# Kernel tuning notes

Hardware: AMD Instinct MI355X
Metric: run time of the kernel (lower is better)

Reference implementation:

```python
import jax, jax.numpy as jnp
import numpy as np

EPS = 1e-5

def conv2d(x, w, b, stride, pad):
    out = jax.lax.conv_general_dilated(x, w, (stride, stride), [(pad, pad), (pad, pad)],
                                       dimension_numbers=('NCHW', 'OIHW', 'NCHW'))
    return out + b[None, :, None, None]

def instance_norm(x):
    # nn.InstanceNorm2d default: affine=False, eps=1e-5, per (N,C) over (H,W)
    m = jnp.mean(x, axis=(2, 3), keepdims=True)
    v = jnp.var(x, axis=(2, 3), keepdims=True)
    return (x - m) * jax.lax.rsqrt(v + EPS)

def deform_conv2d(x, offset, mask, w, b, stride, pad):
    # x: [N,Cin,H,W]; offset: [N,2K,Ho,Wo] as [dy(K);dx(K)]; mask: [N,K,Ho,Wo]
    N, Cin, H, W = x.shape
    Cout, _, kh, kw = w.shape
    K = kh * kw
    Ho, Wo = mask.shape[2], mask.shape[3]
    oy, ox = offset[:, :K], offset[:, K:]
    ky, kx = jnp.meshgrid(jnp.arange(kh), jnp.arange(kw), indexing='ij')
    ky = ky.reshape(K).astype(x.dtype)
    kx = kx.reshape(K).astype(x.dtype)
    base_y = (jnp.arange(Ho) * stride - pad).astype(x.dtype)
    base_x = (jnp.arange(Wo) * stride - pad).astype(x.dtype)
    # sampling coords [N,K,Ho,Wo]
    py = base_y[None, None, :, None] + ky[None, :, None, None] + oy
    px = base_x[None, None, None, :] + kx[None, :, None, None] + ox
    y0 = jnp.floor(py)
    x0 = jnp.floor(px)
    wy = (py - y0)[:, None]  # [N,1,K,Ho,Wo]
    wx = (px - x0)[:, None]
    flat = x.reshape(N, Cin, H * W)

    def sample(yi, xi):
        valid = ((yi >= 0) & (yi <= H - 1) & (xi >= 0) & (xi <= W - 1)).astype(x.dtype)
        yc = jnp.clip(yi, 0, H - 1).astype(jnp.int32)
        xc = jnp.clip(xi, 0, W - 1).astype(jnp.int32)
        idx = yc * W + xc  # [N,K,Ho,Wo]
        vals = jax.vmap(lambda f, i: f[:, i])(flat, idx)  # [N,Cin,K,Ho,Wo]
        return vals * valid[:, None]

    v00 = sample(y0, x0)
    v01 = sample(y0, x0 + 1)
    v10 = sample(y0 + 1, x0)
    v11 = sample(y0 + 1, x0 + 1)
    samp = (v00 * (1 - wy) * (1 - wx) + v01 * (1 - wy) * wx
            + v10 * wy * (1 - wx) + v11 * wy * wx)
    samp = samp * mask[:, None]  # modulated (DCNv2)
    out = jnp.einsum('nckhw,ock->nohw', samp, w.reshape(Cout, Cin, K))
    return out + b[None, :, None, None]

def mdcp(x, off_w, off_b, dcn_w, dcn_b, stride, pad):
    # ModulatedDeformConvPack.forward with input_offset == input_real == x
    o = conv2d(x, off_w, off_b, stride, pad)
    K = o.shape[1] // 3
    o1, o2, m = o[:, :K], o[:, K:2 * K], o[:, 2 * K:]
    offset = jnp.concatenate([o1, o2], axis=1)
    mask = jax.nn.sigmoid(m)
    return deform_conv2d(x, offset, mask, dcn_w, dcn_b, stride, pad)

def res_block(x, w1, b1, w2, b2):
    # MUNIT-style ResBlock: [reflect-pad conv3x3, IN, ReLU] -> [reflect-pad conv3x3, IN] + skip
    h = jnp.pad(x, ((0, 0), (0, 0), (1, 1), (1, 1)), mode='reflect')
    h = jax.nn.relu(instance_norm(conv2d(h, w1, b1, 1, 0)))
    h = jnp.pad(h, ((0, 0), (0, 0), (1, 1), (1, 1)), mode='reflect')
    h = instance_norm(conv2d(h, w2, b2, 1, 0))
    return x + h

def setup_inputs() -> dict:
    key = jax.random.key(0)
    ks = jax.random.split(key, 32)
    N, H, W = 2, 256, 256

    def wconv(k, shape, scale=None):
        if scale is None:
            scale = 1.0 / np.sqrt(shape[1] * shape[2] * shape[3])
        return jax.random.normal(k, shape, jnp.float32) * scale

    def bias(k, n, scale=0.01):
        return jax.random.normal(k, (n,), jnp.float32) * scale

    inp = {}
    inp['x'] = jax.random.normal(ks[0], (N, 3, H, W), jnp.float32)
    # offset/mask convs: small weights (sub-pixel offsets; trained-from-zero in original)
    inp['off1_w'] = wconv(ks[1], (147, 3, 7, 7), 0.01)
    inp['off1_b'] = bias(ks[2], 147)
    inp['dcn1_w'] = wconv(ks[3], (64, 3, 7, 7))
    inp['dcn1_b'] = bias(ks[4], 64)
    inp['off2_w'] = wconv(ks[5], (48, 64, 4, 4), 0.01)
    inp['off2_b'] = bias(ks[6], 48)
    inp['dcn2_w'] = wconv(ks[7], (128, 64, 4, 4))
    inp['dcn2_b'] = bias(ks[8], 128)
    inp['off3_w'] = wconv(ks[9], (48, 128, 4, 4), 0.01)
    inp['off3_b'] = bias(ks[10], 48)
    inp['dcn3_w'] = wconv(ks[11], (256, 128, 4, 4))
    inp['dcn3_b'] = bias(ks[12], 256)
    for i, base in ((1, 13), (2, 17)):
        inp[f'rb{i}_w1'] = wconv(ks[base], (256, 256, 3, 3))
        inp[f'rb{i}_b1'] = bias(ks[base + 1], 256)
        inp[f'rb{i}_w2'] = wconv(ks[base + 2], (256, 256, 3, 3))
        inp[f'rb{i}_b2'] = bias(ks[base + 3], 256)
    return inp

def reference(x, off1_w, off1_b, dcn1_w, dcn1_b, off2_w, off2_b, dcn2_w, dcn2_b,
              off3_w, off3_b, dcn3_w, dcn3_b,
              rb1_w1, rb1_b1, rb1_w2, rb1_b2, rb2_w1, rb2_b1, rb2_w2, rb2_b2):
    h = jax.nn.relu(instance_norm(mdcp(x, off1_w, off1_b, dcn1_w, dcn1_b, 1, 3)))
    skip1 = h
    h = jax.nn.relu(instance_norm(mdcp(h, off2_w, off2_b, dcn2_w, dcn2_b, 2, 1)))
    skip2 = h
    h = jax.nn.relu(instance_norm(mdcp(h, off3_w, off3_b, dcn3_w, dcn3_b, 2, 1)))
    h = res_block(h, rb1_w1, rb1_b1, rb1_w2, rb1_b2)
    h = res_block(h, rb2_w1, rb2_b1, rb2_w2, rb2_b2)
    return (h, skip1, skip2)
```

## Files before the change

kernel.cpp:

```cpp
#include <hip/hip_runtime.h>
#include <hip/hip_bf16.h>
#include <math.h>

#define TPB 256
typedef __hip_bfloat16 bf16;
typedef short bf16x8 __attribute__((ext_vector_type(8)));
typedef float f32x4 __attribute__((ext_vector_type(4)));

constexpr long BIASF  = 0;
constexpr long RB1W1T = 2048;
constexpr long RB1W2T = 591872;
constexpr long RB2W1T = 1181696;
constexpr long RB2W2T = 1771520;
constexpr long FB     = 2361344;
constexpr long WB1OT  = 2361344;
constexpr long WB1DT  = 2382956;
constexpr long WO2T   = 2392364;
constexpr long WB2T   = 2441516;
constexpr long WO3T   = 2572588;
constexpr long WB3T   = 2670892;
constexpr long OFFB   = 3221504;
constexpr long H3F    = 4458496;
constexpr long CLBUF  = 5523456;
constexpr long PST1   = 7620608;
constexpr long PST2   = 7653376;
constexpr long OFF1B = 0,   DCN1B = 147;
constexpr long OFF2B = 211, DCN2B = 259;
constexpr long OFF3B = 387, DCN3B = 435;
constexpr long RB1B1 = 691, RB1B2 = 947;
constexpr long RB2B1 = 1203, RB2B2 = 1459;

template<int BF>
__device__ __forceinline__ float ldT(const void* p, long i) {
    if (BF) {
        unsigned short h = ((const unsigned short*)p)[i];
        return __uint_as_float(((unsigned int)h) << 16);
    }
    return ((const float*)p)[i];
}
template<int BF>
__device__ __forceinline__ void stT(void* p, long i, float v) {
    if (BF) ((bf16*)p)[i] = __float2bfloat16(v);
    else    ((float*)p)[i] = v;
}
__device__ __forceinline__ float bitsToF(unsigned short h) {
    return __uint_as_float(((unsigned int)h) << 16);
}
__device__ __forceinline__ unsigned short fToBits(float v) {
    bf16 h = __float2bfloat16(v);
    return *(unsigned short*)&h;
}

__global__ void detect_kernel(const void* __restrict__ x, int* __restrict__ flag) {
    if (threadIdx.x == 0 && blockIdx.x == 0) {
        const unsigned short* u = (const unsigned short*)x;
        int sane = 0;
        for (int i = 0; i < 256; ++i) {
            float v = bitsToF(u[i]);
            float a = fabsf(v);
            if (a > 0.0009f && a < 1100.f) ++sane;
        }
        *flag = (sane >= 224) ? 1 : 0;
    }
}

struct PtrPack { const void* p[20]; };

template<int BF>
__device__ void repack_all_body(PtrPack pp, float* __restrict__ fw)
{
    constexpr int  bcum  [11] = {0,147,211,259,387,435,691,947,1203,1459,1715};
    int j0 = blockIdx.x * 1024 + threadIdx.x * 4;
    #pragma unroll
    for (int q = 0; q < 4; ++q) {
        int j = j0 + q;
        if (j < 1715) {
            int v = 0;
            #pragma unroll
            for (int s = 1; s < 10; ++s) if (j >= bcum[s]) v = s;
            fw[BIASF + j] = ldT<BF>(pp.p[10 + v], j - bcum[v]);
        }
    }
}
__global__ __launch_bounds__(TPB) void repack_all_kernel(
    PtrPack pp, float* fw, const int* dflag) {
    if (*dflag) repack_all_body<1>(pp, fw);
    else        repack_all_body<0>(pp, fw);
}

__global__ __launch_bounds__(TPB) void repack_dcn_kernel(
    const void* __restrict__ w2, const void* __restrict__ w3,
    const void* __restrict__ w1o, const void* __restrict__ w1d,
    const void* __restrict__ w2o, const void* __restrict__ w3o,
    float* __restrict__ fw, const int* __restrict__ dflag)
{
    int bf = *dflag;
    unsigned short* wb2 = (unsigned short*)(fw + WB2T);
    unsigned short* wb3 = (unsigned short*)(fw + WB3T);
    unsigned short* wb1o = (unsigned short*)(fw + WB1OT);
    unsigned short* wb1d = (unsigned short*)(fw + WB1DT);
    unsigned short* wb2o = (unsigned short*)(fw + WO2T);
    unsigned short* wb3o = (unsigned short*)(fw + WO3T);
    int b = blockIdx.x;
    if (b < 128) {
        int e0 = b * 1024 + threadIdx.x * 4;
        #pragma unroll
        for (int j = 0; j < 4; ++j) {
            int e = e0 + j;
            int co = e >> 10, rem = e & 1023, k = rem >> 6, ci = rem & 63;
            long si = ((long)(co * 64 + ci)) * 16 + k;
            float v = bf ? ldT<1>(w2, si) : ldT<0>(w2, si);
            wb2[e] = fToBits(v);
        }
    } else if (b < 640) {
        int e0 = (b - 128) * 1024 + threadIdx.x * 4;
        #pragma unroll
        for (int j = 0; j < 4; ++j) {
            int e = e0 + j;
            int co = e >> 11, rem = e & 2047, k = rem >> 7, ci = rem & 127;
            long si = ((long)(co * 128 + ci)) * 16 + k;
            float v = bf ? ldT<1>(w3, si) : ldT<0>(w3, si);
            wb3[e] = fToBits(v);
        }
    } else if (b < 665) {
        int e0 = (b - 640) * 1024 + threadIdx.x * 4;
        #pragma unroll
        for (int j = 0; j < 4; ++j) {
            int e = e0 + j;
            int co = e / 160, k = e - co * 160;
            float v = 0.f;
            if (co < 147 && k < 147) {
                long si = (long)co * 147 + k;
                v = bf ? ldT<1>(w1o, si) : ldT<0>(w1o, si);
            }
            wb1o[e] = fToBits(v);
        }
    } else if (b < 675) {
        int e0 = (b - 665) * 1024 + threadIdx.x * 4;
        #pragma unroll
        for (int j = 0; j < 4; ++j) {
            int e = e0 + j;
            int co = e / 160, k = e - co * 160;
            float v = 0.f;
            if (k < 147) {
                long si = (long)co * 147 + k;
                v = bf ? ldT<1>(w1d, si) : ldT<0>(w1d, si);
            }
            wb1d[e] = fToBits(v);
        }
    } else if (b < 739) {
        int e0 = (b - 675) * 1024 + threadIdx.x * 4;
        #pragma unroll
        for (int j = 0; j < 4; ++j) {
            int e = e0 + j;
            int co = e >> 10, rem = e & 1023, k = rem >> 6, ci = rem & 63;
            float v = 0.f;
            if (co < 48) {
                long si = ((long)(co * 64 + ci)) * 16 + k;
                v = bf ? ldT<1>(w2o, si) : ldT<0>(w2o, si);
            }
            wb2o[e] = fToBits(v);
        }
    } else {
        int e0 = (b - 739) * 1024 + threadIdx.x * 4;
        #pragma unroll
        for (int j = 0; j < 4; ++j) {
            int e = e0 + j;
            int co = e >> 11, rem = e & 2047, k = rem >> 7, ci = rem & 127;
            float v = 0.f;
            if (co < 48) {
                long si = ((long)(co * 128 + ci)) * 16 + k;
                v = bf ? ldT<1>(w3o, si) : ldT<0>(w3o, si);
            }
            wb3o[e] = fToBits(v);
        }
    }
}

struct RbPack { const void* src[4]; };
__global__ __launch_bounds__(TPB) void repack_rb_kernel(
    RbPack rp, float* fw, const int* dflag)
{
    __shared__ unsigned short lw[4 * 2304];
    int b = blockIdx.x;
    int ten = b >> 6;
    int co0 = (b & 63) * 4;
    const void* src = rp.src[ten];
    const long dstOff[4] = {RB1W1T, RB1W2T, RB2W1T, RB2W2T};
    unsigned short* dst = (unsigned short*)(fw + dstOff[ten]);
    int bf = *dflag;
    int t = threadIdx.x;
    for (int e = t; e < 4 * 2304; e += TPB) {
        int coL = e / 2304, i = e - coL * 2304;
        long si = (long)(co0 + coL) * 2304 + i;
        float v = bf ? ldT<1>(src, si) : ldT<0>(src, si);
        lw[e] = fToBits(v);
    }
    __syncthreads();
    for (int e = t; e < 9216; e += TPB) {
        int ci = e & 255, coL = (e >> 8) & 3, q = e >> 10;
        dst[((long)q * 256 + co0 + coL) * 256 + ci] = lw[coL * 2304 + ci * 9 + q];
    }
}

template<int BF>
__device__ void x_to_cl4_body(const void* __restrict__ x, unsigned short* __restrict__ x4)
{
    long gid = (long)blockIdx.x * TPB + threadIdx.x;
    int n = (int)(gid >> 16); int p = (int)(gid & 65535);
    long xb = (long)n * 3 * 65536 + p;
    unsigned c0 = fToBits(ldT<BF>(x, xb));
    unsigned c1 = fToBits(ldT<BF>(x, xb + 65536));
    unsigned c2 = fToBits(ldT<BF>(x, xb + 131072));
    uint2 v; v.x = c0 | (c1 << 16); v.y = c2;
    *(uint2*)&x4[gid * 4] = v;
}
__global__ __launch_bounds__(TPB) void x_to_cl4_kernel(
    const void* x, unsigned short* x4, const int* dflag)
{
    if (*dflag) x_to_cl4_body<1>(x, x4);
    else        x_to_cl4_body<0>(x, x4);
}

template<int BF>
__device__ void layer1_mfma_body(
    const unsigned short* __restrict__ x4all, const unsigned short* __restrict__ wo,
    const unsigned short* __restrict__ wd, const float* __restrict__ bias1,
    const float* __restrict__ bias2, void* __restrict__ out, long obase,
    float* xs, unsigned short* A, float* offs)
{
    int b = blockIdx.x;
    int n = b >> 11;
    int ho = (b >> 3) & 255;
    int wo0 = (b & 7) << 5;
    const unsigned short* x4 = x4all + ((long)n << 16) * 4;
    int t = threadIdx.x;

    for (int e = t; e < 7 * 40; e += TPB) {
        int cc = e % 40, rr = e / 40;
        int yy = ho - 3 + rr; int xx = wo0 - 3 + cc;
        float c0 = 0.f, c1 = 0.f, c2 = 0.f;
        if (cc < 38 && yy >= 0 && yy < 256 && xx >= 0 && xx < 256) {
            uint2 v = *(const uint2*)&x4[((long)yy * 256 + xx) * 4];
            c0 = bitsToF((unsigned short)(v.x & 0xffff));
            c1 = bitsToF((unsigned short)(v.x >> 16));
            c2 = bitsToF((unsigned short)(v.y & 0xffff));
        }
        xs[(0 * 7 + rr) * 40 + cc] = c0;
        xs[(1 * 7 + rr) * 40 + cc] = c1;
        xs[(2 * 7 + rr) * 40 + cc] = c2;
    }
    __syncthreads();

    for (int e = t; e < 5120; e += TPB) {
        int kin = e & 31, m = (e >> 5) & 31, kc = e >> 10;
        int k = kc * 32 + kin;
        float v = 0.f;
        if (k < 147) {
            int ci = k / 49, q = k - ci * 49;
            int ky = q / 7, kx = q - ky * 7;
            v = xs[(ci * 7 + ky) * 40 + m + kx];
        }
        A[kc * 1024 + m * 32 + kin] = fToBits(v);
    }
    __syncthreads();

    int wv = t >> 6, lane = t & 63;
    int quad = lane >> 4, l16 = lane & 15;
    int mt = wv & 1, ntb = wv >> 1;

    {
        f32x4 acc[5];
        #pragma unroll
        for (int j = 0; j < 5; ++j) acc[j] = (f32x4){0.f, 0.f, 0.f, 0.f};
        #pragma unroll
        for (int kc = 0; kc < 5; ++kc) {
            bf16x8 a = *(const bf16x8*)&A[(kc * 32 + mt * 16 + l16) * 32 + quad * 8];
            #pragma unroll
            for (int j = 0; j < 5; ++j) {
                int ch = (ntb + 2 * j) * 16 + l16;
                bf16x8 bw = *(const bf16x8*)&wo[ch * 160 + kc * 32 + quad * 8];
                acc[j] = __builtin_amdgcn_mfma_f32_16x16x32_bf16(a, bw, acc[j], 0, 0, 0);
            }
        }
        #pragma unroll
        for (int j = 0; j < 5; ++j) {
            int ch = (ntb + 2 * j) * 16 + l16;
            if (ch < 147) {
                float bv = bias1[ch];
                #pragma unroll
                for (int reg = 0; reg < 4; ++reg) {
                    int m = mt * 16 + quad * 4 + reg;
                    offs[ch * 33 + m] = acc[j][reg] + bv;
                }
            }
        }
    }
    __syncthreads();

    for (int e = t; e < 49 * 32; e += TPB) {
        int p = e & 31; int k = e >> 5;
        float oy = offs[k * 33 + p];
        float ox = offs[(49 + k) * 33 + p];
        float mr = offs[(98 + k) * 33 + p];
        float m = 1.f / (1.f + expf(-mr));
        float py = (float)(ho - 3 + k / 7) + oy;
        float px = (float)(wo0 + p - 3 + k % 7) + ox;
        float y0f = floorf(py), x0f = floorf(px);
        float wy = py - y0f, wx = px - x0f;
        int y0 = (int)y0f, x0 = (int)x0f;
        bool yv0 = (y0 >= 0) && (y0 < 256);
        bool yv1 = (y0 + 1 >= 0) && (y0 + 1 < 256);
        bool xv0 = (x0 >= 0) && (x0 < 256);
        bool xv1 = (x0 + 1 >= 0) && (x0 + 1 < 256);
        int y0c = min(max(y0, 0), 255), y1c = min(max(y0 + 1, 0), 255);
        int x0c = min(max(x0, 0), 255), x1c = min(max(x0 + 1, 0), 255);
        float w00 = (yv0 && xv0) ? (1.f - wy) * (1.f - wx) * m : 0.f;
        float w01 = (yv0 && xv1) ? (1.f - wy) * wx * m : 0.f;
        float w10 = (yv1 && xv0) ? wy * (1.f - wx) * m : 0.f;
        float w11 = (yv1 && xv1) ? wy * wx * m : 0.f;
        uint2 a00 = *(const uint2*)&x4[((long)y0c * 256 + x0c) * 4];
        uint2 a01 = *(const uint2*)&x4[((long)y0c * 256 + x1c) * 4];
        uint2 a10 = *(const uint2*)&x4[((long)y1c * 256 + x0c) * 4];
        uint2 a11 = *(const uint2*)&x4[((long)y1c * 256 + x1c) * 4];
        float s0 = w00 * bitsToF((unsigned short)(a00.x & 0xffff))
                 + w01 * bitsToF((unsigned short)(a01.x & 0xffff))
                 + w10 * bitsToF((unsigned short)(a10.x & 0xffff))
                 + w11 * bitsToF((unsigned short)(a11.x & 0xffff));
        float s1 = w00 * bitsToF((unsigned short)(a00.x >> 16))
                 + w01 * bitsToF((unsigned short)(a01.x >> 16))
                 + w10 * bitsToF((unsigned short)(a10.x >> 16))
                 + w11 * bitsToF((unsigned short)(a11.x >> 16));
        float s2 = w00 * bitsToF((unsigned short)(a00.y & 0xffff))
                 + w01 * bitsToF((unsigned short)(a01.y & 0xffff))
                 + w10 * bitsToF((unsigned short)(a10.y & 0xffff))
                 + w11 * bitsToF((unsigned short)(a11.y & 0xffff));
        offs[k * 33 + p] = s0;
        offs[(49 + k) * 33 + p] = s1;
        offs[(98 + k) * 33 + p] = s2;
    }
    __syncthreads();

    for (int e = t; e < 5120; e += TPB) {
        int kin = e & 31, m = (e >> 5) & 31, kc = e >> 10;
        int k = kc * 32 + kin;
        float v = 0.f;
        if (k < 147) v = offs[k * 33 + m];
        A[kc * 1024 + m * 32 + kin] = fToBits(v);
    }
    __syncthreads();

    f32x4 acc2[2];
    acc2[0] = (f32x4){0.f, 0.f, 0.f, 0.f};
    acc2[1] = (f32x4){0.f, 0.f, 0.f, 0.f};
    #pragma unroll
    for (int kc = 0; kc < 5; ++kc) {
        bf16x8 a = *(const bf16x8*)&A[(kc * 32 + mt * 16 + l16) * 32 + quad * 8];
        #pragma unroll
        for (int j = 0; j < 2; ++j) {
            int co = (ntb + 2 * j) * 16 + l16;
            bf16x8 bw = *(const bf16x8*)&wd[co * 160 + kc * 32 + quad * 8];
            acc2[j] = __builtin_amdgcn_mfma_f32_16x16x32_bf16(a, bw, acc2[j], 0, 0, 0);
        }
    }
    #pragma unroll
    for (int j = 0; j < 2; ++j) {
        int co = (ntb + 2 * j) * 16 + l16;
        float bv = bias2[co];
        #pragma unroll
        for (int reg = 0; reg < 4; ++reg) {
            int wox = wo0 + mt * 16 + quad * 4 + reg;
            long oi = obase + ((long)(n * 64 + co) * 256 + ho) * 256 + wox;
            stT<BF>(out, oi, acc2[j][reg] + bv);
        }
    }
}

__global__ __launch_bounds__(TPB) void layer1_mfma_kernel(
    const unsigned short* x4, const unsigned short* wo, const unsigned short* wd,
    const float* bias1, const float* bias2, void* out, long obase, const int* dflag)
{
    __shared__ __align__(16) float xs[3 * 7 * 40];
    __shared__ __align__(16) unsigned short A[5120];
    __shared__ __align__(16) float offs[147 * 33];
    if (*dflag) layer1_mfma_body<1>(x4, wo, wd, bias1, bias2, out, obase, xs, A, offs);
    else        layer1_mfma_body<0>(x4, wo, wd, bias1, bias2, out, obase, xs, A, offs);
}

template<int CIN, int HH, int WW, int HO, int WO>
__global__ __launch_bounds__(TPB) void offconv_mfma_kernel(
    const unsigned short* __restrict__ xcl, const unsigned short* __restrict__ wb,
    const float* __restrict__ bias_f, float* __restrict__ out)
{
    constexpr int S   = 16 * CIN;
    constexpr int KL  = 512 / CIN;
    constexpr int NCH = 16 / KL;
    constexpr int CH8 = CIN / 8;
    constexpr int UN  = (KL * 16 * CH8) / TPB;
    constexpr int TILES = (HO * WO) / 16;

    __shared__ int tp[256];
    __shared__ __align__(16) unsigned short smp[16 * 512];

    int tile = blockIdx.x % TILES;
    int n    = blockIdx.x / TILES;
    int lp0  = tile * 16;

    {
        int pr = threadIdx.x;
        int k = pr >> 4, p = pr & 15;
        int lp = lp0 + p;
        int ho = lp / WO, wo = lp - ho * WO;
        int yy = ho * 2 - 1 + (k >> 2);
        int xx = wo * 2 - 1 + (k & 3);
        bool valid = (yy >= 0) && (yy < HH) && (xx >= 0) && (xx < WW);
        tp[pr] = valid ? (yy * WW + xx) * CIN : -1;
    }

    int wv = threadIdx.x >> 6, lane = threadIdx.x & 63;
    int quad = lane >> 4, l16 = lane & 15;
    const unsigned short* xn = xcl + (long)n * HH * WW * CIN;

    f32x4 acc = (f32x4){0.f, 0.f, 0.f, 0.f};

    for (int ch = 0; ch < NCH; ++ch) {
        __syncthreads();
        #pragma unroll
        for (int u = 0; u < UN; ++u) {
            int e   = u * TPB + threadIdx.x;
            int prl = e / CH8;
            int ci  = (e - prl * CH8) * 8;
            int pi  = ch * (KL * 16) + prl;
            int kl = prl >> 4, p = prl & 15;
            int t0 = tp[pi];
            uint4 v = {0u, 0u, 0u, 0u};
            if (t0 >= 0) v = *(const uint4*)(xn + t0 + ci);
            int il = kl * CIN + ci;
            *(uint4*)&smp[((il >> 5) * 16 + p) * 32 + (il & 31)] = v;
        }
        __syncthreads();
        #pragma unroll 4
        for (int kk = 0; kk < 16; ++kk) {
            bf16x8 a = *(const bf16x8*)&smp[(kk * 16 + l16) * 32 + quad * 8];
            int co = wv * 16 + l16;
            bf16x8 b = *(const bf16x8*)&wb[(long)co * S + ch * 512 + kk * 32 + quad * 8];
            acc = __builtin_amdgcn_mfma_f32_16x16x32_bf16(a, b, acc, 0, 0, 0);
        }
    }

    int co = wv * 16 + l16;
    if (co < 48) {
        float bv = bias_f[co];
        #pragma unroll
        for (int reg = 0; reg < 4; ++reg) {
            int lp = lp0 + quad * 4 + reg;
            int ho = lp / WO, wo = lp - ho * WO;
            out[((long)(n * 48 + co) * HO + ho) * WO + wo] = acc[reg] + bv;
        }
    }
}

template<int C>
__global__ __launch_bounds__(TPB) void nchw_to_cl_kernel(
    const void* __restrict__ in, long ibase, unsigned short* __restrict__ out,
    int HW, const int* __restrict__ dflag)
{
    __shared__ unsigned short tile[C * 65];
    int bf = *dflag;
    int n   = (blockIdx.x * 64) / HW;
    int px0 = (blockIdx.x * 64) % HW;
    for (int e = threadIdx.x; e < C * 64; e += TPB) {
        int c = e >> 6, p = e & 63;
        long si = ibase + (long)(n * C + c) * HW + px0 + p;
        float v = bf ? ldT<1>(in, si) : ldT<0>(in, si);
        tile[c * 65 + p] = fToBits(v);
    }
    __syncthreads();
    for (int e = threadIdx.x; e < C * 64; e += TPB) {
        int p = e / C, c = e - p * C;
        out[((long)n * HW + px0 + p) * C + c] = tile[c * 65 + p];
    }
}

template<int MODE, int CIN, int COUT, int NWAVES, int HH, int WW, int HO, int WO>
__global__ __launch_bounds__(NWAVES * 64) void deform_mfma_kernel(
    const unsigned short* __restrict__ xcl, const float* __restrict__ off,
    const unsigned short* __restrict__ wb, const float* __restrict__ bias_f,
    void* __restrict__ outp, long obase, const int* __restrict__ dflag)
{
    constexpr int TPBk = NWAVES * 64;
    constexpr int S    = 16 * CIN;
    constexpr int KL   = 512 / CIN;
    constexpr int NCH  = 16 / KL;
    constexpr int CH8  = CIN / 8;
    constexpr int ITER = (KL * 16 * CH8) / TPBk;
    constexpr int TILES = (HO * WO) / 16;

    __shared__ __align__(16) int tpw[256][8];
    __shared__ __align__(16) unsigned short smp[16 * 512];

    int tile = blockIdx.x % TILES;
    int n    = blockIdx.x / TILES;
    int lp0  = tile * 16;
    int tid  = threadIdx.x;

    if (tid < 256) {
        int pr = tid;
        int k = pr >> 4, p = pr & 15;
        int lp = lp0 + p;
        int ho = lp / WO, wo = lp - ho * WO;
        long plane = (long)HO * WO;
        const float* offn = off + (long)n * 48 * plane;
        float oy = offn[(long)k * plane + lp];
        float ox = offn[(long)(16 + k) * plane + lp];
        float mr = offn[(long)(32 + k) * plane + lp];
        float m = 1.f / (1.f + expf(-mr));
        float py = (float)(ho * 2 - 1 + (k >> 2)) + oy;
        float px = (float)(wo * 2 - 1 + (k & 3)) + ox;
        float y0f = floorf(py), x0f = floorf(px);
        float wy = py - y0f, wx = px - x0f;
        int y0 = (int)y0f, x0 = (int)x0f;
        bool yv0 = (y0 >= 0) && (y0 < HH);
        bool yv1 = (y0 + 1 >= 0) && (y0 + 1 < HH);
        bool xv0 = (x0 >= 0) && (x0 < WW);
        bool xv1 = (x0 + 1 >= 0) && (x0 + 1 < WW);
        int y0c = min(max(y0, 0), HH - 1), y1c = min(max(y0 + 1, 0), HH - 1);
        int x0c = min(max(x0, 0), WW - 1), x1c = min(max(x0 + 1, 0), WW - 1);
        tpw[pr][0] = (y0c * WW + x0c) * CIN;
        tpw[pr][1] = (y0c * WW + x1c) * CIN;
        tpw[pr][2] = (y1c * WW + x0c) * CIN;
        tpw[pr][3] = (y1c * WW + x1c) * CIN;
        tpw[pr][4] = __float_as_int((yv0 && xv0) ? (1.f - wy) * (1.f - wx) * m : 0.f);
        tpw[pr][5] = __float_as_int((yv0 && xv1) ? (1.f - wy) * wx * m : 0.f);
        tpw[pr][6] = __float_as_int((yv1 && xv0) ? wy * (1.f - wx) * m : 0.f);
        tpw[pr][7] = __float_as_int((yv1 && xv1) ? wy * wx * m : 0.f);
    }

    int wv = tid >> 6, lane = tid & 63;
    int quad = lane >> 4, l16 = lane & 15;
    int cb = (wv & 3) * 32 + (wv >> 2) * (COUT / 2);
    const unsigned short* xn = xcl + (long)n * HH * WW * CIN;

    f32x4 acc[2];
    acc[0] = (f32x4){0.f, 0.f, 0.f, 0.f};
    acc[1] = (f32x4){0.f, 0.f, 0.f, 0.f};

    for (int ch = 0; ch < NCH; ++ch) {
        __syncthreads();
        #pragma unroll
        for (int it = 0; it < ITER; ++it) {
            int e   = it * TPBk + tid;
            int prl = e / CH8;
            int ci  = (e - prl * CH8) * 8;
            int pi  = ch * (KL * 16) + prl;
            const int4   tp4 = *(const int4*)&tpw[pi][0];
            const float4 tw4 = *(const float4*)&tpw[pi][4];
            uint4 u0 = *(const uint4*)(xn + tp4.x + ci);
            uint4 u1 = *(const uint4*)(xn + tp4.y + ci);
            uint4 u2 = *(const uint4*)(xn + tp4.z + ci);
            uint4 u3 = *(const uint4*)(xn + tp4.w + ci);
            float r[8];
            #pragma unroll
            for (int jj = 0; jj < 8; ++jj) {
                unsigned w0 = ((const unsigned*)&u0)[jj >> 1];
                unsigned w1 = ((const unsigned*)&u1)[jj >> 1];
                unsigned w2 = ((const unsigned*)&u2)[jj >> 1];
                unsigned w3 = ((const unsigned*)&u3)[jj >> 1];
                int sh = (jj & 1) << 4;
                r[jj] = tw4.x * bitsToF((unsigned short)(w0 >> sh))
                      + tw4.y * bitsToF((unsigned short)(w1 >> sh))
                      + tw4.z * bitsToF((unsigned short)(w2 >> sh))
                      + tw4.w * bitsToF((unsigned short)(w3 >> sh));
            }
            uint4 ov;
            ((unsigned*)&ov)[0] = (unsigned)fToBits(r[0]) | ((unsigned)fToBits(r[1]) << 16);
            ((unsigned*)&ov)[1] = (unsigned)fToBits(r[2]) | ((unsigned)fToBits(r[3]) << 16);
            ((unsigned*)&ov)[2] = (unsigned)fToBits(r[4]) | ((unsigned)fToBits(r[5]) << 16);
            ((unsigned*)&ov)[3] = (unsigned)fToBits(r[6]) | ((unsigned)fToBits(r[7]) << 16);
            int il = (prl >> 4) * CIN + ci;
            int p  = prl & 15;
            *(uint4*)&smp[((il >> 5) * 16 + p) * 32 + (il & 31)] = ov;
        }
        __syncthreads();
        #pragma unroll 4
        for (int kk = 0; kk < 16; ++kk) {
            bf16x8 a = *(const bf16x8*)&smp[(kk * 16 + l16) * 32 + quad * 8];
            #pragma unroll
            for (int f = 0; f < 2; ++f) {
                int co = cb + f * 16 + l16;
                bf16x8 b = *(const bf16x8*)&wb[(long)co * S + ch * 512 + kk * 32 + quad * 8];
                acc[f] = __builtin_amdgcn_mfma_f32_16x16x32_bf16(a, b, acc[f], 0, 0, 0);
            }
        }
    }

    if (MODE == 1) {
        unsigned short* oCL = (unsigned short*)outp;
        #pragma unroll
        for (int f = 0; f < 2; ++f) {
            int co = cb + f * 16 + l16;
            float bv = bias_f[co];
            #pragma unroll
            for (int reg = 0; reg < 4; ++reg) {
                int lp = lp0 + quad * 4 + reg;
                oCL[((long)n * HO * WO + lp) * COUT + co] = fToBits(acc[f][reg] + bv);
            }
        }
    } else {
        int bf = *dflag;
        #pragma unroll
        for (int f = 0; f < 2; ++f) {
            int co = cb + f * 16 + l16;
            float bv = bias_f[co];
            #pragma unroll
            for (int reg = 0; reg < 4; ++reg) {
                int lp = lp0 + quad * 4 + reg;
                int ho = lp / WO, wo = lp - ho * WO;
                long oi = obase + ((long)(n * COUT + co) * HO + ho) * WO + wo;
                if (bf) stT<1>(outp, oi, acc[f][reg] + bv);
                else    stT<0>(outp, oi, acc[f][reg] + bv);
            }
        }
    }
}

__global__ __launch_bounds__(TPB) void resconv_mfma_kernel(
    const unsigned short* __restrict__ X, const unsigned short* __restrict__ W,
    const float* __restrict__ bias_f, bf16* __restrict__ Y)
{
    __shared__ __align__(16) unsigned short xs[3 * 66 * 64];
    int b = blockIdx.x;
    int coO = b & 7, r = (b >> 3) & 63, n = b >> 9;
    int t = threadIdx.x;
    int wv = t >> 6;
    int lane = t & 63;
    int quad = lane >> 4, l16 = lane & 15;
    int rows[3];
    rows[0] = (r == 0) ? 1 : r - 1;
    rows[1] = r;
    rows[2] = (r == 63) ? 62 : r + 1;

    f32x4 acc[2];
    acc[0] = (f32x4){0.f, 0.f, 0.f, 0.f};
    acc[1] = (f32x4){0.f, 0.f, 0.f, 0.f};

    long xbase = (long)n * 4096 * 256;

    for (int ci0 = 0; ci0 < 256; ci0 += 64) {
        __syncthreads();
        for (int e = t; e < 3 * 66 * 8; e += TPB) {
            int oct = e & 7;
            int col = (e >> 3) % 66;
            int ky  = e / (66 * 8);
            int gx = col - 1;
            gx = (gx < 0) ? 1 : ((gx > 63) ? 62 : gx);
            bf16x8 v = *(const bf16x8*)&X[xbase + ((long)rows[ky] * 64 + gx) * 256 + ci0 + oct * 8];
            int slot = oct ^ (col & 7);
            *(bf16x8*)&xs[((ky * 66 + col) << 6) + slot * 8] = v;
        }
        __syncthreads();
        #pragma unroll
        for (int q = 0; q < 9; ++q) {
            int ky = q / 3, kx = q % 3;
            int col = wv * 16 + l16 + kx;
            int base = (ky * 66 + col) << 6;
            #pragma unroll
            for (int kh = 0; kh < 2; ++kh) {
                int slot = (kh * 4 + quad) ^ (col & 7);
                bf16x8 a = *(const bf16x8*)&xs[base + slot * 8];
                #pragma unroll
                for (int ct = 0; ct < 2; ++ct) {
                    int co = coO * 32 + ct * 16 + l16;
                    bf16x8 bw = *(const bf16x8*)&W[((long)q * 256 + co) * 256 + ci0 + kh * 32 + quad * 8];
                    acc[ct] = __builtin_amdgcn_mfma_f32_16x16x32_bf16(a, bw, acc[ct], 0, 0, 0);
                }
            }
        }
    }

    long ybase = ((long)n * 4096 + (long)r * 64) * 256;
    #pragma unroll
    for (int ct = 0; ct < 2; ++ct) {
        int co = coO * 32 + ct * 16 + l16;
        float bv = bias_f[co];
        #pragma unroll
        for (int reg = 0; reg < 4; ++reg) {
            int px = wv * 16 + quad * 4 + reg;
            Y[ybase + (long)px * 256 + co] = __float2bfloat16(acc[ct][reg] + bv);
        }
    }
}

__global__ __launch_bounds__(TPB) void cl_stats_kernel(
    const unsigned short* __restrict__ X, float* __restrict__ psum, float* __restrict__ psq)
{
    int blk = blockIdx.x;
    int chunk = blk & 63, n = blk >> 6;
    int co = threadIdx.x;
    float s = 0.f, sq = 0.f;
    const unsigned short* p = X + ((long)n * 4096 + chunk * 64) * 256 + co;
    #pragma unroll 8
    for (int i = 0; i < 64; ++i) {
        float v = bitsToF(p[(long)i * 256]);
        s += v; sq += v * v;
    }
    psum[(n * 64 + chunk) * 256 + co] = s;
    psq [(n * 64 + chunk) * 256 + co] = sq;
}

__device__ __forceinline__ void cl_load_stats(
    const float* psum, const float* psq, int n, float* mv, float* iv)
{
    int t = threadIdx.x;
    float s = 0.f, sq = 0.f;
    #pragma unroll 8
    for (int c = 0; c < 64; ++c) {
        s  += psum[(n * 64 + c) * 256 + t];
        sq += psq [(n * 64 + c) * 256 + t];
    }
    float mean = s / 4096.f;
    mv[t] = mean;
    iv[t] = rsqrtf(sq / 4096.f - mean * mean + 1e-5f);
    __syncthreads();
}

__global__ __launch_bounds__(TPB) void cl_apply_kernel(
    unsigned short* __restrict__ X, const float* __restrict__ psum,
    const float* __restrict__ psq, int relu)
{
    __shared__ float mv[256], iv[256];
    int y = blockIdx.x & 63, n = blockIdx.x >> 6;
    cl_load_stats(psum, psq, n, mv, iv);
    unsigned* row = (unsigned*)(X + ((long)n * 4096 + y * 64) * 256);
    for (int e = threadIdx.x; e < 8192; e += TPB) {
        int co = (e * 2) & 255;
        unsigned u = row[e];
        float v0 = (bitsToF((unsigned short)(u & 0xffff)) - mv[co]) * iv[co];
        float v1 = (bitsToF((unsigned short)(u >> 16)) - mv[co + 1]) * iv[co + 1];
        if (relu) { v0 = fmaxf(v0, 0.f); v1 = fmaxf(v1, 0.f); }
        row[e] = (unsigned)fToBits(v0) | ((unsigned)fToBits(v1) << 16);
    }
}

__global__ __launch_bounds__(TPB) void cl_apply_add_kernel(
    const unsigned short* __restrict__ T, unsigned short* __restrict__ H,
    const float* __restrict__ psum, const float* __restrict__ psq)
{
    __shared__ float mv[256], iv[256];
    int y = blockIdx.x & 63, n = blockIdx.x >> 6;
    cl_load_stats(psum, psq, n, mv, iv);
    long base = ((long)n * 4096 + y * 64) * 256;
    const unsigned* tr = (const unsigned*)(T + base);
    unsigned* hr = (unsigned*)(H + base);
    for (int e = threadIdx.x; e < 8192; e += TPB) {
        int co = (e * 2) & 255;
        unsigned ut = tr[e], uh = hr[e];
        float v0 = bitsToF((unsigned short)(uh & 0xffff))
                 + (bitsToF((unsigned short)(ut & 0xffff)) - mv[co]) * iv[co];
        float v1 = bitsToF((unsigned short)(uh >> 16))
                 + (bitsToF((unsigned short)(ut >> 16)) - mv[co + 1]) * iv[co + 1];
        hr[e] = (unsigned)fToBits(v0) | ((unsigned)fToBits(v1) << 16);
    }
}

__global__ __launch_bounds__(TPB) void cl_apply_final_kernel(
    const unsigned short* __restrict__ T, const unsigned short* __restrict__ H,
    void* __restrict__ outp, const float* __restrict__ psum,
    const float* __restrict__ psq, const int* __restrict__ dflag)
{
    __shared__ float mv[256], iv[256];
    int y = blockIdx.x & 63, n = blockIdx.x >> 6;
    cl_load_stats(psum, psq, n, mv, iv);
    int bf = *dflag;
    int x = threadIdx.x & 63, cg = threadIdx.x >> 6;
    for (int co = cg; co < 256; co += 4) {
        long cli = ((long)(n * 64 + y) * 64 + x) * 256 + co;
        float v = bitsToF(H[cli]) + (bitsToF(T[cli]) - mv[co]) * iv[co];
        long oi = (((long)(n * 256 + co)) * 64 + y) * 64 + x;
        if (bf) ((bf16*)outp)[oi] = __float2bfloat16(v);
        else    ((float*)outp)[oi] = v;
    }
}

__device__ __forceinline__ void reduce2(float& sum, float& sq, float* s1, float* s2)
{
    for (int off = 32; off; off >>= 1) {
        sum += __shfl_down(sum, off, 64);
        sq  += __shfl_down(sq,  off, 64);
    }
    int nw = blockDim.x >> 6;
    int wid = threadIdx.x >> 6;
    if ((threadIdx.x & 63) == 0) { s1[wid] = sum; s2[wid] = sq; }
    __syncthreads();
    sum = 0.f; sq = 0.f;
    for (int w = 0; w < nw; ++w) { sum += s1[w]; sq += s2[w]; }
}

__global__ void instnorm_kernel(
    void* __restrict__ buf, long base0, const int* __restrict__ dflag,
    int HW, int relu)
{
    __shared__ float s1[16], s2[16];
    int bf = *dflag;
    long base = base0 + (long)blockIdx.x * HW;
    float sum = 0.f, sq = 0.f;
    for (int i = threadIdx.x; i < HW; i += blockDim.x) {
        float v = bf ? bitsToF(((const unsigned short*)buf)[base + i])
                     : ((const float*)buf)[base + i];
        sum += v; sq += v * v;
    }
    reduce2(sum, sq, s1, s2);
    float mean = sum / HW;
    float inv = rsqrtf(sq / HW - mean * mean + 1e-5f);
    for (int i = threadIdx.x; i < HW; i += blockDim.x) {
        float v = bf ? bitsToF(((const unsigned short*)buf)[base + i])
                     : ((const float*)buf)[base + i];
        v = (v - mean) * inv;
        if (relu) v = fmaxf(v, 0.f);
        if (bf) ((bf16*)buf)[base + i] = __float2bfloat16(v);
        else    ((float*)buf)[base + i] = v;
    }
}

extern "C" void kernel_launch(void* const* d_in, const int* in_sizes, int n_in,
                              void* d_out, int out_size, void* d_ws, size_t ws_size,
                              hipStream_t stream) {
    const void* x = d_in[0];

    const long SKIP1 = 2097152;
    const long SKIP2 = 10485760;

    int* dflag = (int*)d_ws;
    float* fw = (float*)((char*)d_ws + 64);

    unsigned short* t1 = (unsigned short*)(fw + FB);
    unsigned short* t2 = (unsigned short*)(fw + FB + 1048576);
    unsigned short* h3 = (unsigned short*)(fw + H3F);
    float* offb = fw + OFFB;
    unsigned short* x4 = (unsigned short*)(fw + OFFB);
    float* psum = fw + PST1;
    float* psq  = fw + PST2;
    unsigned short* clbuf = (unsigned short*)(fw + CLBUF);
    const unsigned short* wb1o = (const unsigned short*)(fw + WB1OT);
    const unsigned short* wb1d = (const unsigned short*)(fw + WB1DT);
    const unsigned short* wb2o = (const unsigned short*)(fw + WO2T);
    const unsigned short* wb3o = (const unsigned short*)(fw + WO3T);
    const unsigned short* wb2 = (const unsigned short*)(fw + WB2T);
    const unsigned short* wb3 = (const unsigned short*)(fw + WB3T);
    const unsigned short* rbw1 = (const unsigned short*)(fw + RB1W1T);
    const unsigned short* rbw2 = (const unsigned short*)(fw + RB1W2T);
    const unsigned short* rbw3 = (const unsigned short*)(fw + RB2W1T);
    const unsigned short* rbw4 = (const unsigned short*)(fw + RB2W2T);

    detect_kernel<<<1, 64, 0, stream>>>(x, dflag);

    PtrPack pp;
    for (int i = 0; i < 10; ++i) pp.p[i] = nullptr;
    pp.p[10] = d_in[2];  pp.p[11] = d_in[4];  pp.p[12] = d_in[6];  pp.p[13] = d_in[8];
    pp.p[14] = d_in[10]; pp.p[15] = d_in[12]; pp.p[16] = d_in[14]; pp.p[17] = d_in[16];
    pp.p[18] = d_in[18]; pp.p[19] = d_in[20];
    repack_all_kernel<<<2, TPB, 0, stream>>>(pp, fw, dflag);
    repack_dcn_kernel<<<867, TPB, 0, stream>>>(
        d_in[7], d_in[11], d_in[1], d_in[3], d_in[5], d_in[9], fw, dflag);
    RbPack rp;
    rp.src[0] = d_in[13]; rp.src[1] = d_in[15]; rp.src[2] = d_in[17]; rp.src[3] = d_in[19];
    repack_rb_kernel<<<256, TPB, 0, stream>>>(rp, fw, dflag);

    x_to_cl4_kernel<<<512, TPB, 0, stream>>>(x, x4, dflag);
    layer1_mfma_kernel<<<4096, TPB, 0, stream>>>(
        x4, wb1o, wb1d, fw + OFF1B, fw + DCN1B, d_out, SKIP1, dflag);
    instnorm_kernel<<<128, 1024, 0, stream>>>(d_out, SKIP1, dflag, 65536, 1);
    nchw_to_cl_kernel<64><<<2048, TPB, 0, stream>>>(d_out, SKIP1, clbuf, 65536, dflag);

    offconv_mfma_kernel<64, 256, 256, 128, 128><<<2048, TPB, 0, stream>>>(
        clbuf, wb2o, fw + OFF2B, offb);
    deform_mfma_kernel<0, 64, 128, 4, 256, 256, 128, 128><<<2048, TPB, 0, stream>>>(
        clbuf, offb, wb2, fw + DCN2B, d_out, SKIP2, dflag);
    instnorm_kernel<<<256, 512, 0, stream>>>(d_out, SKIP2, dflag, 16384, 1);
    nchw_to_cl_kernel<128><<<512, TPB, 0, stream>>>(d_out, SKIP2, clbuf, 16384, dflag);

    offconv_mfma_kernel<128, 128, 128, 64, 64><<<512, TPB, 0, stream>>>(
        clbuf, wb3o, fw + OFF3B, offb);
    deform_mfma_kernel<1, 128, 256, 8, 128, 128, 64, 64><<<512, 512, 0, stream>>>(
        clbuf, offb, wb3, fw + DCN3B, h3, 0, dflag);
    cl_stats_kernel<<<128, TPB, 0, stream>>>(h3, psum, psq);
    cl_apply_kernel<<<128, TPB, 0, stream>>>(h3, psum, psq, 1);

    resconv_mfma_kernel<<<1024, TPB, 0, stream>>>(h3, rbw1, fw + RB1B1, (bf16*)t1);
    cl_stats_kernel<<<128, TPB, 0, stream>>>(t1, psum, psq);
    cl_apply_kernel<<<128, TPB, 0, stream>>>(t1, psum, psq, 1);
    resconv_mfma_kernel<<<1024, TPB, 0, stream>>>(t1, rbw2, fw + RB1B2, (bf16*)t2);
    cl_stats_kernel<<<128, TPB, 0, stream>>>(t2, psum, psq);
    cl_apply_add_kernel<<<128, TPB, 0, stream>>>(t2, h3, psum, psq);

    resconv_mfma_kernel<<<1024, TPB, 0, stream>>>(h3, rbw3, fw + RB2B1, (bf16*)t1);
    cl_stats_kernel<<<128, TPB, 0, stream>>>(t1, psum, psq);
    cl_apply_kernel<<<128, TPB, 0, stream>>>(t1, psum, psq, 1);
    resconv_mfma_kernel<<<1024, TPB, 0, stream>>>(t1, rbw4, fw + RB2B2, (bf16*)t2);
    cl_stats_kernel<<<128, TPB, 0, stream>>>(t2, psum, psq);
    cl_apply_final_kernel<<<128, TPB, 0, stream>>>(t2, h3, d_out, psum, psq, dflag);
}
```

Baseline: 843.2 us.

## Split instance-norm into parallel partial stats and fuse apply into NCHW-to-CL transpose

Replaces the monolithic per-channel instance norm kernel, which ran only 128 or 256 blocks, with a chunked statistics kernel that writes 8 partial sums per channel across many more blocks. The normalize+ReLU step is folded into the NCHW-to-channels-last transpose, which now reads the skip tensor once, writes the normalized skip output back in place and fills the CL buffer. This removes one full read/write pass and improves occupancy, at the cost of a partial-sum buffer and per-block recomputation of the channel stats.

```diff
diff --git a/kernel.cpp b/kernel.cpp
--- a/kernel.cpp
+++ b/kernel.cpp
@@ -460,19 +460,69 @@
     }
 }
 
-template<int C>
-__global__ __launch_bounds__(TPB) void nchw_to_cl_kernel(
-    const void* __restrict__ in, long ibase, unsigned short* __restrict__ out,
-    int HW, const int* __restrict__ dflag)
+template<int C, int HW>
+__global__ __launch_bounds__(TPB) void nchw_stats_kernel(
+    const void* __restrict__ buf, long base0, const int* __restrict__ dflag,
+    float* __restrict__ ps1, float* __restrict__ ps2)
+{
+    __shared__ float s1[16], s2[16];
+    constexpr int CH = HW / 8;
+    int b = blockIdx.x;
+    int chunk = b & 7;
+    int nc = b >> 3;
+    int bf = *dflag;
+    long base = base0 + (long)nc * HW + (long)chunk * CH;
+    float sum = 0.f, sq = 0.f;
+    for (int i = threadIdx.x; i < CH; i += TPB) {
+        float v = bf ? bitsToF(((const unsigned short*)buf)[base + i])
+                     : ((const float*)buf)[base + i];
+        sum += v; sq += v * v;
+    }
+    for (int off = 32; off; off >>= 1) {
+        sum += __shfl_down(sum, off, 64);
+        sq  += __shfl_down(sq,  off, 64);
+    }
+    int wid = threadIdx.x >> 6;
+    if ((threadIdx.x & 63) == 0) { s1[wid] = sum; s2[wid] = sq; }
+    __syncthreads();
+    if (threadIdx.x == 0) {
+        float S = 0.f, Q = 0.f;
+        for (int w = 0; w < 4; ++w) { S += s1[w]; Q += s2[w]; }
+        ps1[nc * 8 + chunk] = S;
+        ps2[nc * 8 + chunk] = Q;
+    }
+}
+
+template<int C, int HW>
+__global__ __launch_bounds__(TPB) void nchw_to_cl_norm_kernel(
+    void* __restrict__ buf, long ibase, unsigned short* __restrict__ out,
+    const float* __restrict__ ps1, const float* __restrict__ ps2,
+    const int* __restrict__ dflag)
 {
     __shared__ unsigned short tile[C * 65];
+    __shared__ float mv[C], iv[C];
     int bf = *dflag;
     int n   = (blockIdx.x * 64) / HW;
     int px0 = (blockIdx.x * 64) % HW;
+    if (threadIdx.x < C) {
+        int c = threadIdx.x;
+        float s = 0.f, q = 0.f;
+        #pragma unroll
+        for (int j = 0; j < 8; ++j) {
+            s += ps1[(n * C + c) * 8 + j];
+            q += ps2[(n * C + c) * 8 + j];
+        }
+        float mean = s / (float)HW;
+        mv[c] = mean;
+        iv[c] = rsqrtf(q / (float)HW - mean * mean + 1e-5f);
+    }
+    __syncthreads();
     for (int e = threadIdx.x; e < C * 64; e += TPB) {
         int c = e >> 6, p = e & 63;
         long si = ibase + (long)(n * C + c) * HW + px0 + p;
-        float v = bf ? ldT<1>(in, si) : ldT<0>(in, si);
+        float v = bf ? ldT<1>(buf, si) : ldT<0>(buf, si);
+        v = fmaxf((v - mv[c]) * iv[c], 0.f);
+        if (bf) stT<1>(buf, si, v); else stT<0>(buf, si, v);
         tile[c * 65 + p] = fToBits(v);
     }
     __syncthreads();
@@ -782,46 +832,6 @@
     }
 }
 
-__device__ __forceinline__ void reduce2(float& sum, float& sq, float* s1, float* s2)
-{
-    for (int off = 32; off; off >>= 1) {
-        sum += __shfl_down(sum, off, 64);
-        sq  += __shfl_down(sq,  off, 64);
-    }
-    int nw = blockDim.x >> 6;
-    int wid = threadIdx.x >> 6;
-    if ((threadIdx.x & 63) == 0) { s1[wid] = sum; s2[wid] = sq; }
-    __syncthreads();
-    sum = 0.f; sq = 0.f;
-    for (int w = 0; w < nw; ++w) { sum += s1[w]; sq += s2[w]; }
-}
-
-__global__ void instnorm_kernel(
-    void* __restrict__ buf, long base0, const int* __restrict__ dflag,
-    int HW, int relu)
-{
-    __shared__ float s1[16], s2[16];
-    int bf = *dflag;
-    long base = base0 + (long)blockIdx.x * HW;
-    float sum = 0.f, sq = 0.f;
-    for (int i = threadIdx.x; i < HW; i += blockDim.x) {
-        float v = bf ? bitsToF(((const unsigned short*)buf)[base + i])
-                     : ((const float*)buf)[base + i];
-        sum += v; sq += v * v;
-    }
-    reduce2(sum, sq, s1, s2);
-    float mean = sum / HW;
-    float inv = rsqrtf(sq / HW - mean * mean + 1e-5f);
-    for (int i = threadIdx.x; i < HW; i += blockDim.x) {
-        float v = bf ? bitsToF(((const unsigned short*)buf)[base + i])
-                     : ((const float*)buf)[base + i];
-        v = (v - mean) * inv;
-        if (relu) v = fmaxf(v, 0.f);
-        if (bf) ((bf16*)buf)[base + i] = __float2bfloat16(v);
-        else    ((float*)buf)[base + i] = v;
-    }
-}
-
 extern "C" void kernel_launch(void* const* d_in, const int* in_sizes, int n_in,
                               void* d_out, int out_size, void* d_ws, size_t ws_size,
                               hipStream_t stream) {
@@ -869,15 +879,17 @@
     x_to_cl4_kernel<<<512, TPB, 0, stream>>>(x, x4, dflag);
     layer1_mfma_kernel<<<4096, TPB, 0, stream>>>(
         x4, wb1o, wb1d, fw + OFF1B, fw + DCN1B, d_out, SKIP1, dflag);
-    instnorm_kernel<<<128, 1024, 0, stream>>>(d_out, SKIP1, dflag, 65536, 1);
-    nchw_to_cl_kernel<64><<<2048, TPB, 0, stream>>>(d_out, SKIP1, clbuf, 65536, dflag);
+    nchw_stats_kernel<64, 65536><<<1024, TPB, 0, stream>>>(d_out, SKIP1, dflag, psum, psq);
+    nchw_to_cl_norm_kernel<64, 65536><<<2048, TPB, 0, stream>>>(
+        d_out, SKIP1, clbuf, psum, psq, dflag);
 
     offconv_mfma_kernel<64, 256, 256, 128, 128><<<2048, TPB, 0, stream>>>(
         clbuf, wb2o, fw + OFF2B, offb);
     deform_mfma_kernel<0, 64, 128, 4, 256, 256, 128, 128><<<2048, TPB, 0, stream>>>(
         clbuf, offb, wb2, fw + DCN2B, d_out, SKIP2, dflag);
-    instnorm_kernel<<<256, 512, 0, stream>>>(d_out, SKIP2, dflag, 16384, 1);
-    nchw_to_cl_kernel<128><<<512, TPB, 0, stream>>>(d_out, SKIP2, clbuf, 16384, dflag);
+    nchw_stats_kernel<128, 16384><<<2048, TPB, 0, stream>>>(d_out, SKIP2, dflag, psum, psq);
+    nchw_to_cl_norm_kernel<128, 16384><<<512, TPB, 0, stream>>>(
+        d_out, SKIP2, clbuf, psum, psq, dflag);
 
     offconv_mfma_kernel<128, 128, 128, 64, 64><<<512, TPB, 0, stream>>>(
         clbuf, wb3o, fw + OFF3B, offb);
```

New measurement: 817.8 us. 3.0% less time.
